# Kernel tuning notes

Hardware: AMD Instinct MI355X
Metric: run time of the kernel (lower is better)

The kernel has to match this reference:

```python
import jax, jax.numpy as jnp
import numpy as np

DIM = 512
HEADS = 8
DK = DIM // HEADS
MAX_LEN = 22118
EPS = 1e-5


def _layernorm(h, g, b):
    m = jnp.mean(h, axis=-1, keepdims=True)
    v = jnp.mean((h - m) ** 2, axis=-1, keepdims=True)
    return (h - m) / jnp.sqrt(v + EPS) * g + b


def setup_inputs() -> dict:
    key = jax.random.key(0)
    ks = jax.random.split(key, 16)
    B, S = 4, 2048
    xavier = lambda k, shp: jax.random.normal(k, shp, jnp.float32) * np.sqrt(2.0 / (shp[0] + shp[1]))
    return {
        "x": jax.random.normal(ks[0], (B, S, DIM), jnp.float32),
        "vis_data": jax.random.normal(ks[1], (B, S, DIM), jnp.float32),
        "coord1": jax.random.randint(ks[2], (B, S), 0, MAX_LEN, jnp.int32),
        "coord2": jax.random.randint(ks[3], (B, S), 0, MAX_LEN, jnp.int32),
        "emb1": jax.random.normal(ks[4], (MAX_LEN, DIM // 2), jnp.float32) * 0.02,
        "emb2": jax.random.normal(ks[5], (MAX_LEN, DIM // 2), jnp.float32) * 0.02,
        "wq": xavier(ks[6], (DIM, DIM)), "bq": jnp.zeros((DIM,), jnp.float32),
        "wk": xavier(ks[7], (DIM, DIM)), "bk": jnp.zeros((DIM,), jnp.float32),
        "wv": xavier(ks[8], (DIM, DIM)), "bv": jnp.zeros((DIM,), jnp.float32),
        "w1": xavier(ks[9], (DIM, DIM)), "b1": jnp.zeros((DIM,), jnp.float32),
        "g1": jnp.ones((DIM,), jnp.float32), "beta1": jnp.zeros((DIM,), jnp.float32),
        "w2": xavier(ks[10], (DIM, DIM)), "b2": jnp.zeros((DIM,), jnp.float32),
        "g2": jnp.ones((DIM,), jnp.float32), "beta2": jnp.zeros((DIM,), jnp.float32),
    }


def reference(x, vis_data, coord1, coord2, emb1, emb2, wq, bq, wk, bk, wv, bv,
              w1, b1, g1, beta1, w2, b2, g2, beta2):
    B, S, _ = x.shape
    # learned positional encoding: concat of two coordinate embeddings
    pos = jnp.concatenate([emb1[coord1], emb2[coord2]], axis=-1)  # [B,S,DIM]
    xp = x + pos
    # Q/K from vis_data, V from position-encoded x
    q = (vis_data @ wq + bq).reshape(B, S, HEADS, DK)
    k = (vis_data @ wk + bk).reshape(B, S, HEADS, DK)
    v = (xp @ wv + bv).reshape(B, S, HEADS, DK)
    scores = jnp.einsum("bqhd,bkhd->bhqk", q, k) / np.sqrt(DK).astype(np.float32)
    attn = jax.nn.softmax(scores, axis=-1)  # dropout is identity in eval
    out = jnp.einsum("bhqk,bkhd->bqhd", attn, v).reshape(B, S, DIM)
    # post-attention MLP stack (self.layer)
    h = jax.nn.leaky_relu(out @ w1 + b1, negative_slope=0.2)
    h = _layernorm(h, g1, beta1)
    h = jax.nn.leaky_relu(h @ w2 + b2, negative_slope=0.2)
    h = _layernorm(h, g2, beta2)
    return h
```

## Files before the change

kernel.cpp:

```cpp
#include <hip/hip_runtime.h>

#define DIM 512
#define SEQ 2048
#define MROWS 8192

typedef short short8 __attribute__((ext_vector_type(8)));
typedef float floatx4 __attribute__((ext_vector_type(4)));

__device__ __forceinline__ ushort f2bf(float f) {
  union { float f; unsigned u; } v; v.f = f;
  unsigned r = v.u + 0x7fff + ((v.u >> 16) & 1);
  return (ushort)(r >> 16);
}
__device__ __forceinline__ float bf2f(ushort u) {
  union { unsigned u; float f; } v; v.u = ((unsigned)u) << 16;
  return v.f;
}
__device__ __forceinline__ float fast_exp2(float x) {
  float r;
  asm("v_exp_f32 %0, %1" : "=v"(r) : "v"(x));
  return r;
}

__global__ __launch_bounds__(256) void prep_wtrans_kernel(
    const float* __restrict__ x, const float* __restrict__ vis,
    const int* __restrict__ c1, const int* __restrict__ c2,
    const float* __restrict__ e1, const float* __restrict__ e2,
    const float* __restrict__ wq, const float* __restrict__ wk,
    const float* __restrict__ wv, const float* __restrict__ w1,
    const float* __restrict__ w2,
    ushort* __restrict__ xp_bf, ushort* __restrict__ vis_bf,
    ushort* __restrict__ wt_qkv, ushort* __restrict__ wt1,
    ushort* __restrict__ wt2) {
  __shared__ float Ls[64 * 65];
  if (blockIdx.x < 4096) {
    int gid = blockIdx.x * 256 + threadIdx.x;
    int row = gid >> 7;
    int col = (gid & 127) * 4;
    float4 vv = *(const float4*)(vis + (size_t)row * 512 + col);
    ushort4 vb; vb.x = f2bf(vv.x); vb.y = f2bf(vv.y); vb.z = f2bf(vv.z); vb.w = f2bf(vv.w);
    *(ushort4*)(vis_bf + (size_t)row * 512 + col) = vb;
    float4 p;
    if (col < 256) p = *(const float4*)(e1 + (size_t)c1[row] * 256 + col);
    else           p = *(const float4*)(e2 + (size_t)c2[row] * 256 + col - 256);
    float4 xv = *(const float4*)(x + (size_t)row * 512 + col);
    ushort4 xb; xb.x = f2bf(xv.x + p.x); xb.y = f2bf(xv.y + p.y);
    xb.z = f2bf(xv.z + p.z); xb.w = f2bf(xv.w + p.w);
    *(ushort4*)(xp_bf + (size_t)row * 512 + col) = xb;
  } else {
    int bid = blockIdx.x - 4096;
    int mid = bid >> 6;
    int tile = bid & 63;
    int k0 = (tile >> 3) * 64, n0 = (tile & 7) * 64;
    const float* W = mid == 0 ? wq : mid == 1 ? wk : mid == 2 ? wv : mid == 3 ? w1 : w2;
    ushort* outp = mid < 3 ? (wt_qkv + (size_t)mid * 512 * 512) : (mid == 3 ? wt1 : wt2);
    float scale = (mid == 0) ? 0.125f * 1.44269504f : 1.0f;
    int r = threadIdx.x >> 4, c4 = (threadIdx.x & 15) * 4;
#pragma unroll
    for (int i = 0; i < 4; i++) {
      int row = i * 16 + r;
      float4 wv4 = *(const float4*)(W + (size_t)(k0 + row) * 512 + n0 + c4);
      Ls[row * 65 + c4 + 0] = wv4.x * scale;
      Ls[row * 65 + c4 + 1] = wv4.y * scale;
      Ls[row * 65 + c4 + 2] = wv4.z * scale;
      Ls[row * 65 + c4 + 3] = wv4.w * scale;
    }
    __syncthreads();
    int n = threadIdx.x >> 2, kc = (threadIdx.x & 3) * 16;
    ushort pk[16];
#pragma unroll
    for (int i = 0; i < 16; i++) pk[i] = f2bf(Ls[(kc + i) * 65 + n]);
    ushort* op = outp + (size_t)(n0 + n) * 512 + k0 + kc;
    *(uint4*)op = *(uint4*)pk;
    *(uint4*)(op + 8) = *(uint4*)(pk + 8);
  }
}

template <bool LEAKY>
__global__ __launch_bounds__(256, 4) void gemm_mfma(
    const ushort* __restrict__ A01, const ushort* __restrict__ A2,
    const ushort* __restrict__ Wt,
    const float* __restrict__ bias0, const float* __restrict__ bias1,
    const float* __restrict__ bias2,
    ushort* __restrict__ out0, ushort* __restrict__ out1,
    ushort* __restrict__ out2, float s0scale) {
  __shared__ __align__(16) ushort Sm[24576];
  int t = threadIdx.x;
  int seg = blockIdx.x >> 2;
  int nloc0 = (blockIdx.x & 3) * 128;
  int n0w = blockIdx.x * 128;
  int m0 = blockIdx.y * 64;
  const ushort* A = (seg < 2) ? A01 : A2;
  const float* bias = seg == 0 ? bias0 : seg == 1 ? bias1 : bias2;
  ushort* out = seg == 0 ? out0 : seg == 1 ? out1 : out2;
  float bscale = seg == 0 ? s0scale : 1.0f;

  int w = t >> 6, lane = t & 63;
  int wm = (w & 1) * 32, wn = (w >> 1) * 64;
  int quad = lane >> 4, lcol = lane & 15;
  int l8g = lane >> 3, l7g = lane & 7;
  int gchs = (l7g ^ l8g) * 8;

  floatx4 acc[2][4] = {};

#define GEMM_STAGE(K0, BUF)                                                   \
  {                                                                           \
    ushort* As_ = Sm + (BUF) * 12288;                                         \
    ushort* Bs_ = As_ + 4096;                                                 \
    _Pragma("unroll") for (int i = 0; i < 2; i++) {                           \
      int r0 = w * 16 + i * 8;                                                \
      __builtin_amdgcn_global_load_lds(                                       \
          (const __attribute__((address_space(1))) unsigned*)(                \
              A + (size_t)(m0 + r0 + l8g) * 512 + (K0) + gchs),               \
          (__attribute__((address_space(3))) unsigned*)(&As_[r0 * 64]),       \
          16, 0, 0);                                                          \
    }                                                                         \
    _Pragma("unroll") for (int i = 0; i < 4; i++) {                           \
      int r0 = w * 32 + i * 8;                                                \
      __builtin_amdgcn_global_load_lds(                                       \
          (const __attribute__((address_space(1))) unsigned*)(                \
              Wt + (size_t)(n0w + r0 + l8g) * 512 + (K0) + gchs),             \
          (__attribute__((address_space(3))) unsigned*)(&Bs_[r0 * 64]),       \
          16, 0, 0);                                                          \
    }                                                                         \
  }

  GEMM_STAGE(0, 0);
  asm volatile("s_waitcnt vmcnt(0)" ::: "memory");
  __syncthreads();

  for (int ks = 0; ks < 8; ks++) {
    int cur = ks & 1;
    if (ks < 7) GEMM_STAGE((ks + 1) * 64, cur ^ 1);
    const ushort* As = Sm + cur * 12288;
    const ushort* Bs = As + 4096;
#pragma unroll
    for (int kc = 0; kc < 2; kc++) {
      int pch = ((kc * 4 + quad) ^ (lcol & 7)) * 8;
      short8 af[2], bfr[4];
#pragma unroll
      for (int i = 0; i < 2; i++)
        af[i] = *(const short8*)(&As[(wm + i * 16 + lcol) * 64 + pch]);
#pragma unroll
      for (int i = 0; i < 4; i++)
        bfr[i] = *(const short8*)(&Bs[(wn + i * 16 + lcol) * 64 + pch]);
#pragma unroll
      for (int mt = 0; mt < 2; mt++)
#pragma unroll
        for (int nt = 0; nt < 4; nt++)
          acc[mt][nt] = __builtin_amdgcn_mfma_f32_16x16x32_bf16(
              af[mt], bfr[nt], acc[mt][nt], 0, 0, 0);
    }
    asm volatile("s_waitcnt vmcnt(0)" ::: "memory");
    __syncthreads();
  }
#undef GEMM_STAGE

  float* Ls = (float*)Sm + w * 1088;
  int rr = lane >> 2, cc = (lane & 3) * 16;
#pragma unroll
  for (int mt = 0; mt < 2; mt++) {
#pragma unroll
    for (int nt = 0; nt < 4; nt++) {
      float bv = bias[nloc0 + wn + nt * 16 + lcol] * bscale;
#pragma unroll
      for (int r = 0; r < 4; r++) {
        float vv = acc[mt][nt][r] + bv;
        if (LEAKY) vv = vv >= 0.f ? vv : 0.2f * vv;
        Ls[(quad * 4 + r) * 68 + nt * 16 + lcol] = vv;
      }
    }
    asm volatile("s_waitcnt lgkmcnt(0)" ::: "memory");
    ushort pk[16];
#pragma unroll
    for (int i = 0; i < 16; i += 4) {
      float4 fv = *(const float4*)(&Ls[rr * 68 + cc + i]);
      pk[i] = f2bf(fv.x); pk[i + 1] = f2bf(fv.y);
      pk[i + 2] = f2bf(fv.z); pk[i + 3] = f2bf(fv.w);
    }
    ushort* op = out + (size_t)(m0 + wm + mt * 16 + rr) * 512 + nloc0 + wn + cc;
    *(uint4*)op = *(uint4*)pk;
    *(uint4*)(op + 8) = *(uint4*)(pk + 8);
    asm volatile("s_waitcnt lgkmcnt(0)" ::: "memory");
  }
}

__global__ __launch_bounds__(256, 2) void attn_mfma_kernel(
    const ushort* __restrict__ q, const ushort* __restrict__ k,
    const ushort* __restrict__ v, ushort* __restrict__ out) {
  __shared__ __align__(16) ushort Ks[2][128 * 64];
  __shared__ __align__(16) ushort Vt[2][64 * 128];
  __shared__ __align__(16) unsigned Pp[4096];
  int t = threadIdx.x;
  int blk = blockIdx.x;
  blk = ((blk & 7) << 6) | (blk >> 3);
  int qt = blk & 15, h = (blk >> 4) & 7, b = blk >> 7;
  int wave = t >> 6, lane = t & 63, quad = lane >> 4, lcol = lane & 15;
  int q0 = qt * 128 + wave * 32;
  const size_t base = (size_t)b * SEQ * 512 + h * 64;

  short8 qf[2][2];
#pragma unroll
  for (int qm = 0; qm < 2; qm++)
#pragma unroll
    for (int kc = 0; kc < 2; kc++)
      qf[qm][kc] = *(const short8*)(
          q + base + (size_t)(q0 + qm * 16 + lcol) * 512 + kc * 32 + quad * 8);

  floatx4 O[2][4] = {};
  float lsum[2] = {0.f, 0.f};

  unsigned* Ppw = Pp + wave * 1024;
  int pl = t & 63, dg = t >> 6;
  int l8 = lane >> 3, l7 = lane & 7;
  int kchs = (l7 ^ l8) * 8;
  const ushort* vbase = v + base + (size_t)(2 * pl) * 512 + dg * 16;

  uint4 va[2], vb[2];

#pragma unroll
  for (int j = 0; j < 4; j++) {
    const ushort* gp = k + base + (size_t)((wave * 4 + j) * 8 + l8) * 512 + kchs;
    __builtin_amdgcn_global_load_lds(
        (const __attribute__((address_space(1))) unsigned*)gp,
        (__attribute__((address_space(3))) unsigned*)(&Ks[0][(wave * 4 + j) * 512]),
        16, 0, 0);
  }
  va[0] = *(const uint4*)(vbase);       va[1] = *(const uint4*)(vbase + 8);
  vb[0] = *(const uint4*)(vbase + 512); vb[1] = *(const uint4*)(vbase + 520);
  {
    const ushort* a0 = (const ushort*)va;
    const ushort* a1 = (const ushort*)vb;
#pragma unroll
    for (int i = 0; i < 16; i++) {
      int dim = dg * 16 + i;
      unsigned pack = (unsigned)a0[i] | ((unsigned)a1[i] << 16);
      int pch = (pl >> 2) ^ (dim & 7);
      *(unsigned*)(&Vt[0][dim * 128 + pch * 8 + (pl & 3) * 2]) = pack;
    }
  }
  __syncthreads();

  int cb = 0;
  for (int it = 0; it < 16; it++) {
    if (it < 15) {
      int ktn = (it + 1) * 128;
#pragma unroll
      for (int j = 0; j < 4; j++) {
        const ushort* gp =
            k + base + (size_t)(ktn + (wave * 4 + j) * 8 + l8) * 512 + kchs;
        __builtin_amdgcn_global_load_lds(
            (const __attribute__((address_space(1))) unsigned*)gp,
            (__attribute__((address_space(3))) unsigned*)(
                &Ks[cb ^ 1][(wave * 4 + j) * 512]),
            16, 0, 0);
      }
      const ushort* vr = vbase + (size_t)ktn * 512;
      va[0] = *(const uint4*)(vr);       va[1] = *(const uint4*)(vr + 8);
      vb[0] = *(const uint4*)(vr + 512); vb[1] = *(const uint4*)(vr + 520);
    }

    const ushort* Ksb = Ks[cb];
    const ushort* Vtb = Vt[cb];
#pragma unroll
    for (int half = 0; half < 2; half++) {
      short8 kf[2][4];
#pragma unroll
      for (int kc = 0; kc < 2; kc++) {
        int pch = ((kc * 4 + quad) ^ (lcol & 7)) * 8;
#pragma unroll
        for (int jt = 0; jt < 4; jt++)
          kf[kc][jt] =
              *(const short8*)(&Ksb[((half * 4 + jt) * 16 + lcol) * 64 + pch]);
      }
#pragma unroll
      for (int qm = 0; qm < 2; qm++) {
        floatx4 S[4] = {};
        __builtin_amdgcn_s_setprio(1);
#pragma unroll
        for (int kc = 0; kc < 2; kc++)
#pragma unroll
          for (int jt = 0; jt < 4; jt++)
            S[jt] = __builtin_amdgcn_mfma_f32_16x16x32_bf16(
                kf[kc][jt], qf[qm][kc], S[jt], 0, 0, 0);
        __builtin_amdgcn_s_setprio(0);
#pragma unroll
        for (int jt = 0; jt < 4; jt++) {
          float e0 = fast_exp2(S[jt][0]);
          float e1 = fast_exp2(S[jt][1]);
          float e2 = fast_exp2(S[jt][2]);
          float e3 = fast_exp2(S[jt][3]);
          lsum[qm] += (e0 + e1) + (e2 + e3);
          unsigned p0, p1;
          asm("v_cvt_pk_bf16_f32 %0, %1, %2" : "=v"(p0) : "v"(e0), "v"(e1));
          asm("v_cvt_pk_bf16_f32 %0, %1, %2" : "=v"(p1) : "v"(e2), "v"(e3));
          int c0 = 2 * jt + (quad >> 1);
          uint2 pk2; pk2.x = p0; pk2.y = p1;
          *(uint2*)(Ppw + qm * 512 + lcol * 32 + ((c0 ^ (lcol & 7)) << 2) +
                    (quad & 1) * 2) = pk2;
        }
      }
      asm volatile("s_waitcnt lgkmcnt(0)" ::: "memory");
#pragma unroll
      for (int kc = 0; kc < 2; kc++) {
        short8 vf[4];
        int ch = half * 8 + kc * 4 + quad;
#pragma unroll
        for (int nt = 0; nt < 4; nt++)
          vf[nt] = *(const short8*)(
              &Vtb[(nt * 16 + lcol) * 128 + ((ch ^ (lcol & 7)) * 8)]);
#pragma unroll
        for (int qm = 0; qm < 2; qm++) {
          short8 pf = *(const short8*)(Ppw + qm * 512 + lcol * 32 +
                                       (((kc * 4 + quad) ^ (lcol & 7)) << 2));
          __builtin_amdgcn_s_setprio(1);
#pragma unroll
          for (int nt = 0; nt < 4; nt++)
            O[qm][nt] = __builtin_amdgcn_mfma_f32_16x16x32_bf16(
                vf[nt], pf, O[qm][nt], 0, 0, 0);
          __builtin_amdgcn_s_setprio(0);
        }
      }
    }

    if (it < 15) {
      const ushort* a0 = (const ushort*)va;
      const ushort* a1 = (const ushort*)vb;
      ushort* Vtn = Vt[cb ^ 1];
#pragma unroll
      for (int i = 0; i < 16; i++) {
        int dim = dg * 16 + i;
        unsigned pack = (unsigned)a0[i] | ((unsigned)a1[i] << 16);
        int pch = (pl >> 2) ^ (dim & 7);
        *(unsigned*)(&Vtn[dim * 128 + pch * 8 + (pl & 3) * 2]) = pack;
      }
    }
    asm volatile("s_waitcnt vmcnt(0)" ::: "memory");
    __syncthreads();
    cb ^= 1;
  }

#pragma unroll
  for (int qm = 0; qm < 2; qm++) {
    float s = lsum[qm];
    s += __shfl_xor(s, 16, 64);
    s += __shfl_xor(s, 32, 64);
    float rl = 1.f / s;
#pragma unroll
    for (int nt = 0; nt < 4; nt++) {
      ushort4 o;
      o.x = f2bf(O[qm][nt][0] * rl);
      o.y = f2bf(O[qm][nt][1] * rl);
      o.z = f2bf(O[qm][nt][2] * rl);
      o.w = f2bf(O[qm][nt][3] * rl);
      *(ushort4*)(out + base + (size_t)(q0 + qm * 16 + lcol) * 512 +
                  nt * 16 + quad * 4) = o;
    }
  }
}

template <bool OUTF32>
__global__ __launch_bounds__(256) void ln_kernel(
    const ushort* __restrict__ h, const float* __restrict__ g,
    const float* __restrict__ beta, void* __restrict__ outv) {
  int wave = threadIdx.x >> 6, lane = threadIdx.x & 63;
  int row = blockIdx.x * 4 + wave;
  uint4 raw = *(const uint4*)(h + (size_t)row * 512 + lane * 8);
  const ushort* hu = (const ushort*)&raw;
  float vals[8];
#pragma unroll
  for (int i = 0; i < 8; i++) vals[i] = bf2f(hu[i]);
  float sum = 0.f;
#pragma unroll
  for (int i = 0; i < 8; i++) sum += vals[i];
#pragma unroll
  for (int off = 32; off >= 1; off >>= 1) sum += __shfl_xor(sum, off, 64);
  float mean = sum * (1.f / 512.f);
  float vs = 0.f;
#pragma unroll
  for (int i = 0; i < 8; i++) { float d = vals[i] - mean; vs += d * d; }
#pragma unroll
  for (int off = 32; off >= 1; off >>= 1) vs += __shfl_xor(vs, off, 64);
  float rstd = rsqrtf(vs * (1.f / 512.f) + 1e-5f);
  float4 gv0 = *(const float4*)(g + lane * 8);
  float4 gv1 = *(const float4*)(g + lane * 8 + 4);
  float4 bv0 = *(const float4*)(beta + lane * 8);
  float4 bv1 = *(const float4*)(beta + lane * 8 + 4);
  float gr[8] = {gv0.x, gv0.y, gv0.z, gv0.w, gv1.x, gv1.y, gv1.z, gv1.w};
  float br[8] = {bv0.x, bv0.y, bv0.z, bv0.w, bv1.x, bv1.y, bv1.z, bv1.w};
  float res[8];
#pragma unroll
  for (int i = 0; i < 8; i++) res[i] = (vals[i] - mean) * rstd * gr[i] + br[i];
  if (OUTF32) {
    float* op = (float*)outv + (size_t)row * 512 + lane * 8;
    float4 o0, o1;
    o0.x = res[0]; o0.y = res[1]; o0.z = res[2]; o0.w = res[3];
    o1.x = res[4]; o1.y = res[5]; o1.z = res[6]; o1.w = res[7];
    *(float4*)op = o0; *(float4*)(op + 4) = o1;
  } else {
    ushort* op = (ushort*)outv + (size_t)row * 512 + lane * 8;
    ushort4 o0, o1;
    o0.x = f2bf(res[0]); o0.y = f2bf(res[1]); o0.z = f2bf(res[2]); o0.w = f2bf(res[3]);
    o1.x = f2bf(res[4]); o1.y = f2bf(res[5]); o1.z = f2bf(res[6]); o1.w = f2bf(res[7]);
    *(ushort4*)op = o0; *(ushort4*)(op + 4) = o1;
  }
}

extern "C" void kernel_launch(void* const* d_in, const int* in_sizes, int n_in,
                              void* d_out, int out_size, void* d_ws,
                              size_t ws_size, hipStream_t stream) {
  (void)in_sizes; (void)n_in; (void)out_size; (void)ws_size;
  const float* x     = (const float*)d_in[0];
  const float* vis   = (const float*)d_in[1];
  const int*   c1    = (const int*)d_in[2];
  const int*   c2    = (const int*)d_in[3];
  const float* e1    = (const float*)d_in[4];
  const float* e2    = (const float*)d_in[5];
  const float* wq    = (const float*)d_in[6];
  const float* bq    = (const float*)d_in[7];
  const float* wk    = (const float*)d_in[8];
  const float* bk    = (const float*)d_in[9];
  const float* wv    = (const float*)d_in[10];
  const float* bv    = (const float*)d_in[11];
  const float* w1    = (const float*)d_in[12];
  const float* b1    = (const float*)d_in[13];
  const float* g1    = (const float*)d_in[14];
  const float* beta1 = (const float*)d_in[15];
  const float* w2    = (const float*)d_in[16];
  const float* b2    = (const float*)d_in[17];
  const float* g2    = (const float*)d_in[18];
  const float* beta2 = (const float*)d_in[19];
  float* out = (float*)d_out;
  ushort* ws = (ushort*)d_ws;

  const size_t BUF = (size_t)MROWS * 512;
  ushort* xp_bf  = ws;
  ushort* vis_bf = ws + BUF;
  ushort* q_bf   = ws + 2 * BUF;
  ushort* k_bf   = ws + 3 * BUF;
  ushort* v_bf   = ws + 4 * BUF;
  ushort* wt_qkv = ws + 5 * BUF;
  ushort* wt1    = wt_qkv + 1536 * 512;
  ushort* wt2    = wt1 + 512 * 512;
  ushort* attn_bf = vis_bf;
  ushort* h1_bf   = xp_bf;
  ushort* ln1_bf  = q_bf;
  ushort* h2_bf   = k_bf;

  prep_wtrans_kernel<<<4416, 256, 0, stream>>>(
      x, vis, c1, c2, e1, e2, wq, wk, wv, w1, w2, xp_bf, vis_bf, wt_qkv, wt1, wt2);
  gemm_mfma<false><<<dim3(12, 128), 256, 0, stream>>>(
      vis_bf, xp_bf, wt_qkv, bq, bk, bv, q_bf, k_bf, v_bf, 0.125f * 1.44269504f);
  attn_mfma_kernel<<<512, 256, 0, stream>>>(q_bf, k_bf, v_bf, attn_bf);
  gemm_mfma<true><<<dim3(4, 128), 256, 0, stream>>>(
      attn_bf, attn_bf, wt1, b1, b1, b1, h1_bf, h1_bf, h1_bf, 1.0f);
  ln_kernel<false><<<2048, 256, 0, stream>>>(h1_bf, g1, beta1, ln1_bf);
  gemm_mfma<true><<<dim3(4, 128), 256, 0, stream>>>(
      ln1_bf, ln1_bf, wt2, b2, b2, b2, h2_bf, h2_bf, h2_bf, 1.0f);
  ln_kernel<true><<<2048, 256, 0, stream>>>(h2_bf, g2, beta2, out);
}
```

Measured before the change: 258.3 us.

## Shrink attention tiles to 64 queries and 64 keys, double grid and occupancy

```diff
diff --git a/kernel.cpp b/kernel.cpp
--- a/kernel.cpp
+++ b/kernel.cpp
@@ -185,177 +185,152 @@
   }
 }
 
-__global__ __launch_bounds__(256, 2) void attn_mfma_kernel(
+__global__ __launch_bounds__(256, 4) void attn_mfma_kernel(
     const ushort* __restrict__ q, const ushort* __restrict__ k,
     const ushort* __restrict__ v, ushort* __restrict__ out) {
-  __shared__ __align__(16) ushort Ks[2][128 * 64];
-  __shared__ __align__(16) ushort Vt[2][64 * 128];
-  __shared__ __align__(16) unsigned Pp[4096];
+  __shared__ __align__(16) ushort Ks[2][64 * 64];
+  __shared__ __align__(16) ushort Vt[2][64 * 64];
+  __shared__ __align__(16) unsigned Pp[2048];
   int t = threadIdx.x;
   int blk = blockIdx.x;
-  blk = ((blk & 7) << 6) | (blk >> 3);
-  int qt = blk & 15, h = (blk >> 4) & 7, b = blk >> 7;
+  blk = ((blk & 7) << 7) | (blk >> 3);
+  int qt = blk & 31, h = (blk >> 5) & 7, b = blk >> 8;
   int wave = t >> 6, lane = t & 63, quad = lane >> 4, lcol = lane & 15;
-  int q0 = qt * 128 + wave * 32;
+  int q0 = qt * 64 + wave * 16;
   const size_t base = (size_t)b * SEQ * 512 + h * 64;
 
-  short8 qf[2][2];
-#pragma unroll
-  for (int qm = 0; qm < 2; qm++)
-#pragma unroll
-    for (int kc = 0; kc < 2; kc++)
-      qf[qm][kc] = *(const short8*)(
-          q + base + (size_t)(q0 + qm * 16 + lcol) * 512 + kc * 32 + quad * 8);
-
-  floatx4 O[2][4] = {};
-  float lsum[2] = {0.f, 0.f};
-
-  unsigned* Ppw = Pp + wave * 1024;
-  int pl = t & 63, dg = t >> 6;
+  short8 qf[2];
+#pragma unroll
+  for (int kc = 0; kc < 2; kc++)
+    qf[kc] = *(const short8*)(
+        q + base + (size_t)(q0 + lcol) * 512 + kc * 32 + quad * 8);
+
+  floatx4 O[4] = {};
+  float lsum = 0.f;
+
+  unsigned* Ppw = Pp + wave * 512;
   int l8 = lane >> 3, l7 = lane & 7;
   int kchs = (l7 ^ l8) * 8;
-  const ushort* vbase = v + base + (size_t)(2 * pl) * 512 + dg * 16;
-
-  uint4 va[2], vb[2];
-
-#pragma unroll
-  for (int j = 0; j < 4; j++) {
-    const ushort* gp = k + base + (size_t)((wave * 4 + j) * 8 + l8) * 512 + kchs;
-    __builtin_amdgcn_global_load_lds(
-        (const __attribute__((address_space(1))) unsigned*)gp,
-        (__attribute__((address_space(3))) unsigned*)(&Ks[0][(wave * 4 + j) * 512]),
-        16, 0, 0);
-  }
-  va[0] = *(const uint4*)(vbase);       va[1] = *(const uint4*)(vbase + 8);
-  vb[0] = *(const uint4*)(vbase + 512); vb[1] = *(const uint4*)(vbase + 520);
+  int krow = wave * 8 + l8;
+  int vp = t & 31, vdg = t >> 5;
+  const ushort* vbase = v + base + (size_t)(2 * vp) * 512 + vdg * 8;
+
+  uint4 ka0, ka1, va, vb;
+
+  ka0 = *(const uint4*)(k + base + (size_t)krow * 512 + kchs);
+  ka1 = *(const uint4*)(k + base + (size_t)(krow + 32) * 512 + kchs);
+  va = *(const uint4*)vbase;
+  vb = *(const uint4*)(vbase + 512);
+  *(uint4*)(&Ks[0][krow * 64 + l7 * 8]) = ka0;
+  *(uint4*)(&Ks[0][(krow + 32) * 64 + l7 * 8]) = ka1;
   {
-    const ushort* a0 = (const ushort*)va;
-    const ushort* a1 = (const ushort*)vb;
-#pragma unroll
-    for (int i = 0; i < 16; i++) {
-      int dim = dg * 16 + i;
+    const ushort* a0 = (const ushort*)&va;
+    const ushort* a1 = (const ushort*)&vb;
+#pragma unroll
+    for (int i = 0; i < 8; i++) {
+      int dim = vdg * 8 + i;
       unsigned pack = (unsigned)a0[i] | ((unsigned)a1[i] << 16);
-      int pch = (pl >> 2) ^ (dim & 7);
-      *(unsigned*)(&Vt[0][dim * 128 + pch * 8 + (pl & 3) * 2]) = pack;
+      *(unsigned*)(&Vt[0][dim * 64 + ((vp >> 2) ^ (dim & 7)) * 8 +
+                          (vp & 3) * 2]) = pack;
     }
   }
   __syncthreads();
 
   int cb = 0;
-  for (int it = 0; it < 16; it++) {
-    if (it < 15) {
-      int ktn = (it + 1) * 128;
-#pragma unroll
-      for (int j = 0; j < 4; j++) {
-        const ushort* gp =
-            k + base + (size_t)(ktn + (wave * 4 + j) * 8 + l8) * 512 + kchs;
-        __builtin_amdgcn_global_load_lds(
-            (const __attribute__((address_space(1))) unsigned*)gp,
-            (__attribute__((address_space(3))) unsigned*)(
-                &Ks[cb ^ 1][(wave * 4 + j) * 512]),
-            16, 0, 0);
-      }
+  for (int it = 0; it < 32; it++) {
+    if (it < 31) {
+      int ktn = (it + 1) * 64;
+      ka0 = *(const uint4*)(k + base + (size_t)(ktn + krow) * 512 + kchs);
+      ka1 = *(const uint4*)(k + base + (size_t)(ktn + krow + 32) * 512 + kchs);
       const ushort* vr = vbase + (size_t)ktn * 512;
-      va[0] = *(const uint4*)(vr);       va[1] = *(const uint4*)(vr + 8);
-      vb[0] = *(const uint4*)(vr + 512); vb[1] = *(const uint4*)(vr + 520);
+      va = *(const uint4*)vr;
+      vb = *(const uint4*)(vr + 512);
     }
 
     const ushort* Ksb = Ks[cb];
     const ushort* Vtb = Vt[cb];
-#pragma unroll
-    for (int half = 0; half < 2; half++) {
-      short8 kf[2][4];
-#pragma unroll
-      for (int kc = 0; kc < 2; kc++) {
-        int pch = ((kc * 4 + quad) ^ (lcol & 7)) * 8;
-#pragma unroll
-        for (int jt = 0; jt < 4; jt++)
-          kf[kc][jt] =
-              *(const short8*)(&Ksb[((half * 4 + jt) * 16 + lcol) * 64 + pch]);
+
+    short8 kf[2][4];
+#pragma unroll
+    for (int kc = 0; kc < 2; kc++) {
+      int pch = ((kc * 4 + quad) ^ l7) * 8;
+#pragma unroll
+      for (int jt = 0; jt < 4; jt++)
+        kf[kc][jt] = *(const short8*)(&Ksb[(jt * 16 + lcol) * 64 + pch]);
+    }
+    floatx4 S[4] = {};
+    __builtin_amdgcn_s_setprio(1);
+#pragma unroll
+    for (int kc = 0; kc < 2; kc++)
+#pragma unroll
+      for (int jt = 0; jt < 4; jt++)
+        S[jt] = __builtin_amdgcn_mfma_f32_16x16x32_bf16(
+            kf[kc][jt], qf[kc], S[jt], 0, 0, 0);
+    __builtin_amdgcn_s_setprio(0);
+
+#pragma unroll
+    for (int jt = 0; jt < 4; jt++) {
+      float e0 = fast_exp2(S[jt][0]);
+      float e1 = fast_exp2(S[jt][1]);
+      float e2 = fast_exp2(S[jt][2]);
+      float e3 = fast_exp2(S[jt][3]);
+      lsum += (e0 + e1) + (e2 + e3);
+      unsigned p0, p1;
+      asm("v_cvt_pk_bf16_f32 %0, %1, %2" : "=v"(p0) : "v"(e0), "v"(e1));
+      asm("v_cvt_pk_bf16_f32 %0, %1, %2" : "=v"(p1) : "v"(e2), "v"(e3));
+      int c0 = 2 * jt + (quad >> 1);
+      uint2 pk2; pk2.x = p0; pk2.y = p1;
+      *(uint2*)(Ppw + lcol * 32 + ((c0 ^ l7) << 2) + (quad & 1) * 2) = pk2;
+    }
+    asm volatile("s_waitcnt lgkmcnt(0)" ::: "memory");
+
+#pragma unroll
+    for (int kc = 0; kc < 2; kc++) {
+      short8 vf[4];
+      int ch = ((kc * 4 + quad) ^ l7) * 8;
+#pragma unroll
+      for (int nt = 0; nt < 4; nt++)
+        vf[nt] = *(const short8*)(&Vtb[(nt * 16 + lcol) * 64 + ch]);
+      short8 pf = *(const short8*)(Ppw + lcol * 32 +
+                                   (((kc * 4 + quad) ^ l7) << 2));
+      __builtin_amdgcn_s_setprio(1);
+#pragma unroll
+      for (int nt = 0; nt < 4; nt++)
+        O[nt] = __builtin_amdgcn_mfma_f32_16x16x32_bf16(
+            vf[nt], pf, O[nt], 0, 0, 0);
+      __builtin_amdgcn_s_setprio(0);
+    }
+
+    if (it < 31) {
+      ushort* Ksn = Ks[cb ^ 1];
+      *(uint4*)(&Ksn[krow * 64 + l7 * 8]) = ka0;
+      *(uint4*)(&Ksn[(krow + 32) * 64 + l7 * 8]) = ka1;
+      const ushort* a0 = (const ushort*)&va;
+      const ushort* a1 = (const ushort*)&vb;
+      ushort* Vtn = Vt[cb ^ 1];
+#pragma unroll
+      for (int i = 0; i < 8; i++) {
+        int dim = vdg * 8 + i;
+        unsigned pack = (unsigned)a0[i] | ((unsigned)a1[i] << 16);
+        *(unsigned*)(&Vtn[dim * 64 + ((vp >> 2) ^ (dim & 7)) * 8 +
+                          (vp & 3) * 2]) = pack;
       }
-#pragma unroll
-      for (int qm = 0; qm < 2; qm++) {
-        floatx4 S[4] = {};
-        __builtin_amdgcn_s_setprio(1);
-#pragma unroll
-        for (int kc = 0; kc < 2; kc++)
-#pragma unroll
-          for (int jt = 0; jt < 4; jt++)
-            S[jt] = __builtin_amdgcn_mfma_f32_16x16x32_bf16(
-                kf[kc][jt], qf[qm][kc], S[jt], 0, 0, 0);
-        __builtin_amdgcn_s_setprio(0);
-#pragma unroll
-        for (int jt = 0; jt < 4; jt++) {
-          float e0 = fast_exp2(S[jt][0]);
-          float e1 = fast_exp2(S[jt][1]);
-          float e2 = fast_exp2(S[jt][2]);
-          float e3 = fast_exp2(S[jt][3]);
-          lsum[qm] += (e0 + e1) + (e2 + e3);
-          unsigned p0, p1;
-          asm("v_cvt_pk_bf16_f32 %0, %1, %2" : "=v"(p0) : "v"(e0), "v"(e1));
-          asm("v_cvt_pk_bf16_f32 %0, %1, %2" : "=v"(p1) : "v"(e2), "v"(e3));
-          int c0 = 2 * jt + (quad >> 1);
-          uint2 pk2; pk2.x = p0; pk2.y = p1;
-          *(uint2*)(Ppw + qm * 512 + lcol * 32 + ((c0 ^ (lcol & 7)) << 2) +
-                    (quad & 1) * 2) = pk2;
-        }
-      }
-      asm volatile("s_waitcnt lgkmcnt(0)" ::: "memory");
-#pragma unroll
-      for (int kc = 0; kc < 2; kc++) {
-        short8 vf[4];
-        int ch = half * 8 + kc * 4 + quad;
-#pragma unroll
-        for (int nt = 0; nt < 4; nt++)
-          vf[nt] = *(const short8*)(
-              &Vtb[(nt * 16 + lcol) * 128 + ((ch ^ (lcol & 7)) * 8)]);
-#pragma unroll
-        for (int qm = 0; qm < 2; qm++) {
-          short8 pf = *(const short8*)(Ppw + qm * 512 + lcol * 32 +
-                                       (((kc * 4 + quad) ^ (lcol & 7)) << 2));
-          __builtin_amdgcn_s_setprio(1);
-#pragma unroll
-          for (int nt = 0; nt < 4; nt++)
-            O[qm][nt] = __builtin_amdgcn_mfma_f32_16x16x32_bf16(
-                vf[nt], pf, O[qm][nt], 0, 0, 0);
-          __builtin_amdgcn_s_setprio(0);
-        }
-      }
-    }
-
-    if (it < 15) {
-      const ushort* a0 = (const ushort*)va;
-      const ushort* a1 = (const ushort*)vb;
-      ushort* Vtn = Vt[cb ^ 1];
-#pragma unroll
-      for (int i = 0; i < 16; i++) {
-        int dim = dg * 16 + i;
-        unsigned pack = (unsigned)a0[i] | ((unsigned)a1[i] << 16);
-        int pch = (pl >> 2) ^ (dim & 7);
-        *(unsigned*)(&Vtn[dim * 128 + pch * 8 + (pl & 3) * 2]) = pack;
-      }
-    }
-    asm volatile("s_waitcnt vmcnt(0)" ::: "memory");
+    }
     __syncthreads();
     cb ^= 1;
   }
 
-#pragma unroll
-  for (int qm = 0; qm < 2; qm++) {
-    float s = lsum[qm];
-    s += __shfl_xor(s, 16, 64);
-    s += __shfl_xor(s, 32, 64);
-    float rl = 1.f / s;
-#pragma unroll
-    for (int nt = 0; nt < 4; nt++) {
-      ushort4 o;
-      o.x = f2bf(O[qm][nt][0] * rl);
-      o.y = f2bf(O[qm][nt][1] * rl);
-      o.z = f2bf(O[qm][nt][2] * rl);
-      o.w = f2bf(O[qm][nt][3] * rl);
-      *(ushort4*)(out + base + (size_t)(q0 + qm * 16 + lcol) * 512 +
-                  nt * 16 + quad * 4) = o;
-    }
+  lsum += __shfl_xor(lsum, 16, 64);
+  lsum += __shfl_xor(lsum, 32, 64);
+  float rl = 1.f / lsum;
+#pragma unroll
+  for (int nt = 0; nt < 4; nt++) {
+    ushort4 o;
+    o.x = f2bf(O[nt][0] * rl);
+    o.y = f2bf(O[nt][1] * rl);
+    o.z = f2bf(O[nt][2] * rl);
+    o.w = f2bf(O[nt][3] * rl);
+    *(ushort4*)(out + base + (size_t)(q0 + lcol) * 512 + nt * 16 + quad * 4) = o;
   }
 }
 
@@ -451,7 +426,7 @@
       x, vis, c1, c2, e1, e2, wq, wk, wv, w1, w2, xp_bf, vis_bf, wt_qkv, wt1, wt2);
   gemm_mfma<false><<<dim3(12, 128), 256, 0, stream>>>(
       vis_bf, xp_bf, wt_qkv, bq, bk, bv, q_bf, k_bf, v_bf, 0.125f * 1.44269504f);
-  attn_mfma_kernel<<<512, 256, 0, stream>>>(q_bf, k_bf, v_bf, attn_bf);
+  attn_mfma_kernel<<<1024, 256, 0, stream>>>(q_bf, k_bf, v_bf, attn_bf);
   gemm_mfma<true><<<dim3(4, 128), 256, 0, stream>>>(
       attn_bf, attn_bf, wt1, b1, b1, b1, h1_bf, h1_bf, h1_bf, 1.0f);
   ln_kernel<false><<<2048, 256, 0, stream>>>(h1_bf, g1, beta1, ln1_bf);
```

Result: faster. 248.2 us (-3.9%).
